# Performance work log

Hardware: AMD Instinct MI355X
Metric: run time of the kernel (lower is better)

## Reference

```python
import jax, jax.numpy as jnp
import numpy as np

N_NODES = 100000
N_EDGES = 3200000
IN_DIM, HID, OUT = 5, 64, 2


def _gcn_conv(x, W, b, src, dst):
    """PyG GCNConv: out = D^-1/2 (A + I) D^-1/2 (x W) + b.
    src/dst are edge_index[0]/edge_index[1] (source_to_target flow)."""
    n = x.shape[0]
    h = x @ W  # [N, out]
    # degree including self loop: deg[i] = 1 + #edges with dst == i
    deg = jnp.ones((n,), h.dtype).at[dst].add(1.0)
    inv_sqrt = jax.lax.rsqrt(deg)
    coef = inv_sqrt[src] * inv_sqrt[dst]  # [E]
    msgs = h[src] * coef[:, None]  # [E, out] gather
    agg = jax.ops.segment_sum(msgs, dst, num_segments=n)  # scatter-add
    # self-loop contribution: norm = inv_sqrt[i]^2 = 1/deg[i]
    agg = agg + h * (1.0 / deg)[:, None]
    return agg + b


def setup_inputs() -> dict:
    key = jax.random.key(0)
    ks = jax.random.split(key, 8)
    x = jax.random.normal(ks[0], (N_NODES, IN_DIM), dtype=jnp.float32)
    edge_index = jax.random.randint(ks[1], (2, N_EDGES), 0, N_NODES, dtype=jnp.int32)
    def glorot(k, fan_in, fan_out):
        lim = np.sqrt(6.0 / (fan_in + fan_out)).astype(np.float32)
        return jax.random.uniform(k, (fan_in, fan_out), jnp.float32, -lim, lim)
    return {
        "x": x,
        "edge_index": edge_index,
        "W1": glorot(ks[2], IN_DIM, HID), "b1": jnp.zeros((HID,), jnp.float32),
        "W2": glorot(ks[3], HID, HID),    "b2": jnp.zeros((HID,), jnp.float32),
        "W3": glorot(ks[4], HID, OUT),    "b3": jnp.zeros((OUT,), jnp.float32),
    }


def reference(x, edge_index, W1, b1, W2, b2, W3, b3):
    src, dst = edge_index[0], edge_index[1]
    # eval mode: dropout is identity
    h = jax.nn.relu(_gcn_conv(x, W1, b1, src, dst))
    h = jax.nn.relu(_gcn_conv(h, W2, b2, src, dst))
    return _gcn_conv(h, W3, b3, src, dst)
```

## Files before the change

### kernel.cpp

```cpp
#include <hip/hip_runtime.h>

#define CB 256
#define MAXNB 1024


__global__ void k_hist(const int* __restrict__ dst, int* __restrict__ histG,
                       int E, int NB, int chunk) {
  __shared__ int hist[MAXNB];
  int b = blockIdx.x, tid = threadIdx.x;
  for (int k = tid; k < NB; k += 256) hist[k] = 0;
  __syncthreads();
  int beg = b * chunk, end = min(E, beg + chunk);
  for (int i = beg + tid; i < end; i += 256) atomicAdd(&hist[dst[i] >> 8], 1);
  __syncthreads();
  for (int k = tid; k < NB; k += 256) histG[(size_t)k * CB + b] = hist[k];
}

__global__ void k_scan_local(const int* __restrict__ in, int* __restrict__ out,
                             int* __restrict__ blockSums, int n) {
  __shared__ int wsum[16];
  __shared__ int wpre[16];
  int tid = threadIdx.x;
  int gid = blockIdx.x * 1024 + tid;
  int v = (gid < n) ? in[gid] : 0;
  int lane = tid & 63, wv = tid >> 6;
  int x = v;
#pragma unroll
  for (int d = 1; d < 64; d <<= 1) {
    int t = __shfl_up(x, d);
    if (lane >= d) x += t;
  }
  if (lane == 63) wsum[wv] = x;
  __syncthreads();
  if (tid == 0) {
    int run = 0;
#pragma unroll
    for (int i = 0; i < 16; ++i) { wpre[i] = run; run += wsum[i]; }
    blockSums[blockIdx.x] = run;
  }
  __syncthreads();
  if (gid < n) out[gid] = x - v + wpre[wv];
}

__global__ void k_scan_blocks(const int* __restrict__ blockSums, int* __restrict__ blockOffs, int nb) {
  __shared__ int wtot[4];
  int tid = threadIdx.x;
  int lane = tid & 63, w = tid >> 6;
  int v = (tid < nb) ? blockSums[tid] : 0;
  int x = v;
#pragma unroll
  for (int d = 1; d < 64; d <<= 1) {
    int t = __shfl_up(x, d);
    if (lane >= d) x += t;
  }
  if (lane == 63) wtot[w] = x;
  __syncthreads();
  int pre = 0;
  for (int i = 0; i < w; ++i) pre += wtot[i];
  int ex = x - v + pre;
  if (tid < nb) blockOffs[tid] = ex;
  if (tid == nb - 1) blockOffs[nb] = ex + v;
}

__global__ void k_scatter(const int* __restrict__ src, const int* __restrict__ dst,
                          const int* __restrict__ histS, const int* __restrict__ blockOffs,
                          unsigned* __restrict__ recs, int E, int NB, int chunk) {
  __shared__ int cur[MAXNB];
  int b = blockIdx.x, tid = threadIdx.x;
  for (int k = tid; k < NB; k += 256) {
    int gid = k * CB + b;
    cur[k] = histS[gid] + blockOffs[gid >> 10];
  }
  __syncthreads();
  int beg = b * chunk, end = min(E, beg + chunk);
  for (int i = beg + tid; i < end; i += 256) {
    int s = src[i], d = dst[i];
    int pos = atomicAdd(&cur[d >> 8], 1);
    recs[pos] = ((unsigned)s << 8) | (unsigned)(d & 255);
  }
}

__global__ void k_build(const unsigned* __restrict__ recs, const int* __restrict__ histS,
                        const int* __restrict__ blockOffs,
                        int* __restrict__ offs, float* __restrict__ inv_sqrt,
                        int* __restrict__ srcs, int N, int NB, int E) {
  __shared__ int cnt[256];
  __shared__ int cur[256];
  __shared__ int wtot[4];
  int k = blockIdx.x, tid = threadIdx.x;
  int g0 = k * CB;
  int ebeg = histS[g0] + blockOffs[g0 >> 10];
  int eend = E;
  if (k + 1 < NB) {
    int g1 = (k + 1) * CB;
    eend = histS[g1] + blockOffs[g1 >> 10];
  }
  cnt[tid] = 0;
  __syncthreads();
  for (int i = ebeg + tid; i < eend; i += 256) atomicAdd(&cnt[recs[i] & 255u], 1);
  __syncthreads();
  int v = cnt[tid];
  int lane = tid & 63, w = tid >> 6;
  int x = v;
#pragma unroll
  for (int d = 1; d < 64; d <<= 1) {
    int t = __shfl_up(x, d);
    if (lane >= d) x += t;
  }
  if (lane == 63) wtot[w] = x;
  __syncthreads();
  int pre = 0;
  for (int i = 0; i < w; ++i) pre += wtot[i];
  int gpos = ebeg + (x - v) + pre;
  int node = k * 256 + tid;
  if (node < N) {
    offs[node] = gpos;
    inv_sqrt[node] = rsqrtf(1.0f + (float)v);
  }
  cur[tid] = gpos;
  if (k == NB - 1 && tid == 0) offs[N] = E;
  __syncthreads();
  for (int i = ebeg + tid; i < eend; i += 256) {
    unsigned r = recs[i];
    int pos = atomicAdd(&cur[r & 255u], 1);
    srcs[pos] = (int)(r >> 8);
  }
}


__global__ void k_l12(const float* __restrict__ x, const int* __restrict__ offs,
                      const int* __restrict__ srcs, const float* __restrict__ inv_sqrt,
                      const float* __restrict__ W1, const float* __restrict__ b1,
                      const float* __restrict__ W2, float* __restrict__ h2raw, int n) {
  __shared__ float hrow[4][2][64];
  int tid = threadIdx.x;
  int lane = tid & 63, w = tid >> 6;
  int hl = lane & 31, half = lane >> 5;
  float w1r[5];
#pragma unroll
  for (int k = 0; k < 5; ++k) w1r[k] = W1[k * 64 + lane];
  float bias = b1[lane];
  float wreg[64];
#pragma unroll
  for (int k = 0; k < 64; ++k) wreg[k] = W2[k * 64 + lane];
  float* slotA = &hrow[w][0][0];
  float* slotB = &hrow[w][1][0];
  int wid0 = (blockIdx.x * blockDim.x + tid) >> 6;
  int nw = (gridDim.x * blockDim.x) >> 6;
  for (int i2 = wid0 * 2; i2 < n; i2 += nw * 2) {
    int iA = i2, iB = i2 + 1;
    int node = (half == 0) ? iA : iB;
    bool valid = node < n;
    float a0 = 0.f, a1 = 0.f, a2 = 0.f, a3 = 0.f, a4 = 0.f;
    float isd = 0.f;
    if (valid) {
      isd = inv_sqrt[node];
      int beg = offs[node], end = offs[node + 1];
      for (int j = beg + hl; j < end; j += 32) {
        int s = srcs[j];
        float c = inv_sqrt[s] * isd;
        const float* xs = x + (size_t)s * 5;
        float4 xv = *(const float4*)xs;
        float x4 = xs[4];
        a0 = fmaf(xv.x, c, a0); a1 = fmaf(xv.y, c, a1); a2 = fmaf(xv.z, c, a2);
        a3 = fmaf(xv.w, c, a3); a4 = fmaf(x4, c, a4);
      }
    }
#pragma unroll
    for (int d = 16; d; d >>= 1) {
      a0 += __shfl_xor(a0, d); a1 += __shfl_xor(a1, d); a2 += __shfl_xor(a2, d);
      a3 += __shfl_xor(a3, d); a4 += __shfl_xor(a4, d);
    }
    if (valid) {
      float sc = isd * isd;
      const float* xi = x + (size_t)node * 5;
      a0 = fmaf(xi[0], sc, a0); a1 = fmaf(xi[1], sc, a1); a2 = fmaf(xi[2], sc, a2);
      a3 = fmaf(xi[3], sc, a3); a4 = fmaf(xi[4], sc, a4);
    }
    float aA0 = __shfl(a0, hl),      aA1 = __shfl(a1, hl),      aA2 = __shfl(a2, hl);
    float aA3 = __shfl(a3, hl),      aA4 = __shfl(a4, hl);
    float aB0 = __shfl(a0, hl | 32), aB1 = __shfl(a1, hl | 32), aB2 = __shfl(a2, hl | 32);
    float aB3 = __shfl(a3, hl | 32), aB4 = __shfl(a4, hl | 32);
    float hA = bias;
    hA = fmaf(aA0, w1r[0], hA); hA = fmaf(aA1, w1r[1], hA); hA = fmaf(aA2, w1r[2], hA);
    hA = fmaf(aA3, w1r[3], hA); hA = fmaf(aA4, w1r[4], hA);
    hA = fmaxf(hA, 0.f);
    float hB = bias;
    hB = fmaf(aB0, w1r[0], hB); hB = fmaf(aB1, w1r[1], hB); hB = fmaf(aB2, w1r[2], hB);
    hB = fmaf(aB3, w1r[3], hB); hB = fmaf(aB4, w1r[4], hB);
    hB = fmaxf(hB, 0.f);
    slotA[lane] = hA;
    slotB[lane] = hB;
    float ac0 = 0.f, ac1 = 0.f, ac2 = 0.f, ac3 = 0.f;
#pragma unroll
    for (int k4 = 0; k4 < 16; ++k4) {
      float4 hq = *(const float4*)&slotA[k4 * 4];
      ac0 = fmaf(hq.x, wreg[k4 * 4],     ac0);
      ac1 = fmaf(hq.y, wreg[k4 * 4 + 1], ac1);
      ac2 = fmaf(hq.z, wreg[k4 * 4 + 2], ac2);
      ac3 = fmaf(hq.w, wreg[k4 * 4 + 3], ac3);
    }
    h2raw[(size_t)iA * 64 + lane] = (ac0 + ac1) + (ac2 + ac3);
    if (iB < n) {
      float bc0 = 0.f, bc1 = 0.f, bc2 = 0.f, bc3 = 0.f;
#pragma unroll
      for (int k4 = 0; k4 < 16; ++k4) {
        float4 hq = *(const float4*)&slotB[k4 * 4];
        bc0 = fmaf(hq.x, wreg[k4 * 4],     bc0);
        bc1 = fmaf(hq.y, wreg[k4 * 4 + 1], bc1);
        bc2 = fmaf(hq.z, wreg[k4 * 4 + 2], bc2);
        bc3 = fmaf(hq.w, wreg[k4 * 4 + 3], bc3);
      }
      h2raw[(size_t)iB * 64 + lane] = (bc0 + bc1) + (bc2 + bc3);
    }
  }
}

__global__ void k_agg64w3(const float* __restrict__ hraw, const int* __restrict__ offs,
                          const int* __restrict__ srcs, const float* __restrict__ inv_sqrt,
                          const float* __restrict__ b2, const float* __restrict__ W3,
                          float* __restrict__ h3, int n) {
  int wid = (blockIdx.x * blockDim.x + threadIdx.x) >> 6;
  int lane = threadIdx.x & 63;
  if (wid >= n) return;
  int sub = lane >> 4;
  int fl  = lane & 15;
  float w30[4], w31[4];
#pragma unroll
  for (int q = 0; q < 4; ++q) {
    w30[q] = W3[(fl * 4 + q) * 2];
    w31[q] = W3[(fl * 4 + q) * 2 + 1];
  }
  int beg = offs[wid], end = offs[wid + 1];
  float isd = inv_sqrt[wid];
  float ax0 = 0.f, ay0 = 0.f, az0 = 0.f, aw0 = 0.f;
  float ax1 = 0.f, ay1 = 0.f, az1 = 0.f, aw1 = 0.f;
  int j = beg + sub;
  for (; j + 12 < end; j += 16) {
    int s0 = srcs[j], s1 = srcs[j + 4], s2 = srcs[j + 8], s3 = srcs[j + 12];
    float c0 = inv_sqrt[s0] * isd, c1 = inv_sqrt[s1] * isd;
    float c2 = inv_sqrt[s2] * isd, c3 = inv_sqrt[s3] * isd;
    float4 r0 = *(const float4*)(hraw + (size_t)s0 * 64 + fl * 4);
    float4 r1 = *(const float4*)(hraw + (size_t)s1 * 64 + fl * 4);
    float4 r2 = *(const float4*)(hraw + (size_t)s2 * 64 + fl * 4);
    float4 r3 = *(const float4*)(hraw + (size_t)s3 * 64 + fl * 4);
    ax0 = fmaf(r0.x, c0, ax0); ay0 = fmaf(r0.y, c0, ay0);
    az0 = fmaf(r0.z, c0, az0); aw0 = fmaf(r0.w, c0, aw0);
    ax1 = fmaf(r1.x, c1, ax1); ay1 = fmaf(r1.y, c1, ay1);
    az1 = fmaf(r1.z, c1, az1); aw1 = fmaf(r1.w, c1, aw1);
    ax0 = fmaf(r2.x, c2, ax0); ay0 = fmaf(r2.y, c2, ay0);
    az0 = fmaf(r2.z, c2, az0); aw0 = fmaf(r2.w, c2, aw0);
    ax1 = fmaf(r3.x, c3, ax1); ay1 = fmaf(r3.y, c3, ay1);
    az1 = fmaf(r3.z, c3, az1); aw1 = fmaf(r3.w, c3, aw1);
  }
  for (; j < end; j += 4) {
    int s0 = srcs[j];
    float c0 = inv_sqrt[s0] * isd;
    float4 r0 = *(const float4*)(hraw + (size_t)s0 * 64 + fl * 4);
    ax0 = fmaf(r0.x, c0, ax0); ay0 = fmaf(r0.y, c0, ay0);
    az0 = fmaf(r0.z, c0, az0); aw0 = fmaf(r0.w, c0, aw0);
  }
  float ax = ax0 + ax1, ay = ay0 + ay1, az = az0 + az1, aw = aw0 + aw1;
  ax += __shfl_xor(ax, 16); ay += __shfl_xor(ay, 16);
  az += __shfl_xor(az, 16); aw += __shfl_xor(aw, 16);
  ax += __shfl_xor(ax, 32); ay += __shfl_xor(ay, 32);
  az += __shfl_xor(az, 32); aw += __shfl_xor(aw, 32);
  float sc = isd * isd;
  float4 self = *(const float4*)(hraw + (size_t)wid * 64 + fl * 4);
  float4 bb   = *(const float4*)(b2 + fl * 4);
  float hx = fmaxf(ax + self.x * sc + bb.x, 0.f);
  float hy = fmaxf(ay + self.y * sc + bb.y, 0.f);
  float hz = fmaxf(az + self.z * sc + bb.z, 0.f);
  float hw = fmaxf(aw + self.w * sc + bb.w, 0.f);
  float p0 = hx * w30[0] + hy * w30[1] + hz * w30[2] + hw * w30[3];
  float p1 = hx * w31[0] + hy * w31[1] + hz * w31[2] + hw * w31[3];
#pragma unroll
  for (int d = 8; d; d >>= 1) { p0 += __shfl_xor(p0, d); p1 += __shfl_xor(p1, d); }
  if (lane == 0) {
    h3[(size_t)wid * 2]     = p0;
    h3[(size_t)wid * 2 + 1] = p1;
  }
}

__global__ void k_agg2(const float* __restrict__ h3, const int* __restrict__ offs,
                       const int* __restrict__ srcs, const float* __restrict__ inv_sqrt,
                       const float* __restrict__ b3, float* __restrict__ out, int n) {
  int wid = (blockIdx.x * blockDim.x + threadIdx.x) >> 6;
  int lane = threadIdx.x & 63;
  if (wid >= n) return;
  int beg = offs[wid], end = offs[wid + 1];
  float isd = inv_sqrt[wid];
  float a0 = 0.f, a1 = 0.f;
  for (int j = beg + lane; j < end; j += 64) {
    int s = srcs[j];
    float c = inv_sqrt[s] * isd;
    a0 = fmaf(h3[(size_t)s * 2], c, a0);
    a1 = fmaf(h3[(size_t)s * 2 + 1], c, a1);
  }
#pragma unroll
  for (int d = 32; d; d >>= 1) { a0 += __shfl_xor(a0, d); a1 += __shfl_xor(a1, d); }
  if (lane == 0) {
    float sc = isd * isd;
    out[(size_t)wid * 2]     = a0 + h3[(size_t)wid * 2] * sc + b3[0];
    out[(size_t)wid * 2 + 1] = a1 + h3[(size_t)wid * 2 + 1] * sc + b3[1];
  }
}


extern "C" void kernel_launch(void* const* d_in, const int* in_sizes, int n_in,
                              void* d_out, int out_size, void* d_ws, size_t ws_size,
                              hipStream_t stream) {
  const float* x  = (const float*)d_in[0];
  const int*   ei = (const int*)d_in[1];
  const float* W1 = (const float*)d_in[2];
  const float* b1 = (const float*)d_in[3];
  const float* W2 = (const float*)d_in[4];
  const float* b2 = (const float*)d_in[5];
  const float* W3 = (const float*)d_in[6];
  const float* b3 = (const float*)d_in[7];
  float* out = (float*)d_out;

  const int N = in_sizes[0] / 5;
  const int E = in_sizes[1] / 2;
  const int* src = ei;
  const int* dst = ei + E;

  const int NB = (N + 255) >> 8;
  const int chunk = (E + CB - 1) / CB;
  const int n2 = NB * CB;
  const int nb2 = (n2 + 1023) / 1024;

  char* p = (char*)d_ws;
  auto alloc = [&](size_t bytes) {
    char* r = p;
    p += (bytes + 255) & ~(size_t)255;
    return r;
  };
  int*      histG     = (int*)alloc((size_t)n2 * 4);
  int*      histS     = (int*)alloc((size_t)n2 * 4);
  int*      blockSums = (int*)alloc((size_t)nb2 * 4);
  int*      blockOffs = (int*)alloc((size_t)(nb2 + 1) * 4);
  unsigned* recs      = (unsigned*)alloc((size_t)E * 4);
  int*      srcs      = (int*)alloc((size_t)E * 4);
  int*      offs      = (int*)alloc((size_t)(N + 1) * 4);
  float*    inv_sqrt  = (float*)alloc((size_t)N * 4);
  float*    hB        = (float*)alloc((size_t)N * 64 * 4);
  float*    h3        = (float*)alloc((size_t)N * 2 * 4);

  const int wavesBlocks = (N * 64 + 255) / 256;

  k_hist<<<CB, 256, 0, stream>>>(dst, histG, E, NB, chunk);
  k_scan_local<<<nb2, 1024, 0, stream>>>(histG, histS, blockSums, n2);
  k_scan_blocks<<<1, 256, 0, stream>>>(blockSums, blockOffs, nb2);
  k_scatter<<<CB, 256, 0, stream>>>(src, dst, histS, blockOffs, recs, E, NB, chunk);
  k_build<<<NB, 256, 0, stream>>>(recs, histS, blockOffs, offs, inv_sqrt, srcs, N, NB, E);

  k_l12<<<2048, 256, 0, stream>>>(x, offs, srcs, inv_sqrt, W1, b1, W2, hB, N);
  k_agg64w3<<<wavesBlocks, 256, 0, stream>>>(hB, offs, srcs, inv_sqrt, b2, W3, h3, N);
  k_agg2<<<wavesBlocks, 256, 0, stream>>>(h3, offs, srcs, inv_sqrt, b3, out, N);
}
```

Baseline: 263.7 us.

## Pre-scale features by inv_sqrt and slice 64-wide hidden layer for aggregation

Source features are pre-multiplied by inv_sqrt(deg) in the build and GEMM epilogues, which removes the per-edge gather of inv_sqrt[s] in every aggregation. The 64-wide hidden layer is stored as eight feature slices of 8 floats each, and each block aggregates one slice. This keeps the gathered working set per slice small enough to stay cache-resident. Partial W3 projections per slice are then summed in a new small kernel. This adds an extra launch and a partial buffer, and the slice kernel reads srcs eight times.

```diff
diff --git a/kernel.cpp b/kernel.cpp
--- a/kernel.cpp
+++ b/kernel.cpp
@@ -81,9 +81,10 @@
 }
 
 __global__ void k_build(const unsigned* __restrict__ recs, const int* __restrict__ histS,
-                        const int* __restrict__ blockOffs,
+                        const int* __restrict__ blockOffs, const float* __restrict__ x,
                         int* __restrict__ offs, float* __restrict__ inv_sqrt,
-                        int* __restrict__ srcs, int N, int NB, int E) {
+                        float* __restrict__ xp, int* __restrict__ srcs,
+                        int N, int NB, int E) {
   __shared__ int cnt[256];
   __shared__ int cur[256];
   __shared__ int wtot[4];
@@ -101,21 +102,26 @@
   __syncthreads();
   int v = cnt[tid];
   int lane = tid & 63, w = tid >> 6;
-  int x = v;
+  int x_ = v;
 #pragma unroll
   for (int d = 1; d < 64; d <<= 1) {
-    int t = __shfl_up(x, d);
-    if (lane >= d) x += t;
-  }
-  if (lane == 63) wtot[w] = x;
+    int t = __shfl_up(x_, d);
+    if (lane >= d) x_ += t;
+  }
+  if (lane == 63) wtot[w] = x_;
   __syncthreads();
   int pre = 0;
   for (int i = 0; i < w; ++i) pre += wtot[i];
-  int gpos = ebeg + (x - v) + pre;
+  int gpos = ebeg + (x_ - v) + pre;
   int node = k * 256 + tid;
   if (node < N) {
     offs[node] = gpos;
-    inv_sqrt[node] = rsqrtf(1.0f + (float)v);
+    float is = rsqrtf(1.0f + (float)v);
+    inv_sqrt[node] = is;
+    const float* xr = x + (size_t)node * 5;
+    float* xo = xp + (size_t)node * 5;
+    xo[0] = xr[0] * is; xo[1] = xr[1] * is; xo[2] = xr[2] * is;
+    xo[3] = xr[3] * is; xo[4] = xr[4] * is;
   }
   cur[tid] = gpos;
   if (k == NB - 1 && tid == 0) offs[N] = E;
@@ -128,14 +134,15 @@
 }
 
 
-__global__ void k_l12(const float* __restrict__ x, const int* __restrict__ offs,
+__global__ void k_l12(const float* __restrict__ xp, const int* __restrict__ offs,
                       const int* __restrict__ srcs, const float* __restrict__ inv_sqrt,
                       const float* __restrict__ W1, const float* __restrict__ b1,
-                      const float* __restrict__ W2, float* __restrict__ h2raw, int n) {
+                      const float* __restrict__ W2, float* __restrict__ hS, int n) {
   __shared__ float hrow[4][2][64];
   int tid = threadIdx.x;
   int lane = tid & 63, w = tid >> 6;
   int hl = lane & 31, half = lane >> 5;
+  int slice = lane >> 3, feat = lane & 7;
   float w1r[5];
 #pragma unroll
   for (int k = 0; k < 5; ++k) w1r[k] = W1[k * 64 + lane];
@@ -158,12 +165,10 @@
       int beg = offs[node], end = offs[node + 1];
       for (int j = beg + hl; j < end; j += 32) {
         int s = srcs[j];
-        float c = inv_sqrt[s] * isd;
-        const float* xs = x + (size_t)s * 5;
+        const float* xs = xp + (size_t)s * 5;
         float4 xv = *(const float4*)xs;
         float x4 = xs[4];
-        a0 = fmaf(xv.x, c, a0); a1 = fmaf(xv.y, c, a1); a2 = fmaf(xv.z, c, a2);
-        a3 = fmaf(xv.w, c, a3); a4 = fmaf(x4, c, a4);
+        a0 += xv.x; a1 += xv.y; a2 += xv.z; a3 += xv.w; a4 += x4;
       }
     }
 #pragma unroll
@@ -172,15 +177,15 @@
       a3 += __shfl_xor(a3, d); a4 += __shfl_xor(a4, d);
     }
     if (valid) {
-      float sc = isd * isd;
-      const float* xi = x + (size_t)node * 5;
-      a0 = fmaf(xi[0], sc, a0); a1 = fmaf(xi[1], sc, a1); a2 = fmaf(xi[2], sc, a2);
-      a3 = fmaf(xi[3], sc, a3); a4 = fmaf(xi[4], sc, a4);
+      const float* xi = xp + (size_t)node * 5;
+      a0 = (a0 + xi[0]) * isd; a1 = (a1 + xi[1]) * isd; a2 = (a2 + xi[2]) * isd;
+      a3 = (a3 + xi[3]) * isd; a4 = (a4 + xi[4]) * isd;
     }
     float aA0 = __shfl(a0, hl),      aA1 = __shfl(a1, hl),      aA2 = __shfl(a2, hl);
     float aA3 = __shfl(a3, hl),      aA4 = __shfl(a4, hl);
     float aB0 = __shfl(a0, hl | 32), aB1 = __shfl(a1, hl | 32), aB2 = __shfl(a2, hl | 32);
     float aB3 = __shfl(a3, hl | 32), aB4 = __shfl(a4, hl | 32);
+    float isdA = __shfl(isd, 0), isdB = __shfl(isd, 32);
     float hA = bias;
     hA = fmaf(aA0, w1r[0], hA); hA = fmaf(aA1, w1r[1], hA); hA = fmaf(aA2, w1r[2], hA);
     hA = fmaf(aA3, w1r[3], hA); hA = fmaf(aA4, w1r[4], hA);
@@ -200,7 +205,7 @@
       ac2 = fmaf(hq.z, wreg[k4 * 4 + 2], ac2);
       ac3 = fmaf(hq.w, wreg[k4 * 4 + 3], ac3);
     }
-    h2raw[(size_t)iA * 64 + lane] = (ac0 + ac1) + (ac2 + ac3);
+    hS[((size_t)slice * n + iA) * 8 + feat] = ((ac0 + ac1) + (ac2 + ac3)) * isdA;
     if (iB < n) {
       float bc0 = 0.f, bc1 = 0.f, bc2 = 0.f, bc3 = 0.f;
 #pragma unroll
@@ -211,98 +216,86 @@
         bc2 = fmaf(hq.z, wreg[k4 * 4 + 2], bc2);
         bc3 = fmaf(hq.w, wreg[k4 * 4 + 3], bc3);
       }
-      h2raw[(size_t)iB * 64 + lane] = (bc0 + bc1) + (bc2 + bc3);
-    }
-  }
-}
-
-__global__ void k_agg64w3(const float* __restrict__ hraw, const int* __restrict__ offs,
-                          const int* __restrict__ srcs, const float* __restrict__ inv_sqrt,
-                          const float* __restrict__ b2, const float* __restrict__ W3,
-                          float* __restrict__ h3, int n) {
-  int wid = (blockIdx.x * blockDim.x + threadIdx.x) >> 6;
-  int lane = threadIdx.x & 63;
-  if (wid >= n) return;
-  int sub = lane >> 4;
-  int fl  = lane & 15;
-  float w30[4], w31[4];
-#pragma unroll
-  for (int q = 0; q < 4; ++q) {
-    w30[q] = W3[(fl * 4 + q) * 2];
-    w31[q] = W3[(fl * 4 + q) * 2 + 1];
-  }
-  int beg = offs[wid], end = offs[wid + 1];
-  float isd = inv_sqrt[wid];
-  float ax0 = 0.f, ay0 = 0.f, az0 = 0.f, aw0 = 0.f;
-  float ax1 = 0.f, ay1 = 0.f, az1 = 0.f, aw1 = 0.f;
-  int j = beg + sub;
-  for (; j + 12 < end; j += 16) {
-    int s0 = srcs[j], s1 = srcs[j + 4], s2 = srcs[j + 8], s3 = srcs[j + 12];
-    float c0 = inv_sqrt[s0] * isd, c1 = inv_sqrt[s1] * isd;
-    float c2 = inv_sqrt[s2] * isd, c3 = inv_sqrt[s3] * isd;
-    float4 r0 = *(const float4*)(hraw + (size_t)s0 * 64 + fl * 4);
-    float4 r1 = *(const float4*)(hraw + (size_t)s1 * 64 + fl * 4);
-    float4 r2 = *(const float4*)(hraw + (size_t)s2 * 64 + fl * 4);
-    float4 r3 = *(const float4*)(hraw + (size_t)s3 * 64 + fl * 4);
-    ax0 = fmaf(r0.x, c0, ax0); ay0 = fmaf(r0.y, c0, ay0);
-    az0 = fmaf(r0.z, c0, az0); aw0 = fmaf(r0.w, c0, aw0);
-    ax1 = fmaf(r1.x, c1, ax1); ay1 = fmaf(r1.y, c1, ay1);
-    az1 = fmaf(r1.z, c1, az1); aw1 = fmaf(r1.w, c1, aw1);
-    ax0 = fmaf(r2.x, c2, ax0); ay0 = fmaf(r2.y, c2, ay0);
-    az0 = fmaf(r2.z, c2, az0); aw0 = fmaf(r2.w, c2, aw0);
-    ax1 = fmaf(r3.x, c3, ax1); ay1 = fmaf(r3.y, c3, ay1);
-    az1 = fmaf(r3.z, c3, az1); aw1 = fmaf(r3.w, c3, aw1);
-  }
-  for (; j < end; j += 4) {
-    int s0 = srcs[j];
-    float c0 = inv_sqrt[s0] * isd;
-    float4 r0 = *(const float4*)(hraw + (size_t)s0 * 64 + fl * 4);
-    ax0 = fmaf(r0.x, c0, ax0); ay0 = fmaf(r0.y, c0, ay0);
-    az0 = fmaf(r0.z, c0, az0); aw0 = fmaf(r0.w, c0, aw0);
-  }
-  float ax = ax0 + ax1, ay = ay0 + ay1, az = az0 + az1, aw = aw0 + aw1;
-  ax += __shfl_xor(ax, 16); ay += __shfl_xor(ay, 16);
-  az += __shfl_xor(az, 16); aw += __shfl_xor(aw, 16);
-  ax += __shfl_xor(ax, 32); ay += __shfl_xor(ay, 32);
-  az += __shfl_xor(az, 32); aw += __shfl_xor(aw, 32);
-  float sc = isd * isd;
-  float4 self = *(const float4*)(hraw + (size_t)wid * 64 + fl * 4);
-  float4 bb   = *(const float4*)(b2 + fl * 4);
-  float hx = fmaxf(ax + self.x * sc + bb.x, 0.f);
-  float hy = fmaxf(ay + self.y * sc + bb.y, 0.f);
-  float hz = fmaxf(az + self.z * sc + bb.z, 0.f);
-  float hw = fmaxf(aw + self.w * sc + bb.w, 0.f);
-  float p0 = hx * w30[0] + hy * w30[1] + hz * w30[2] + hw * w30[3];
-  float p1 = hx * w31[0] + hy * w31[1] + hz * w31[2] + hw * w31[3];
-#pragma unroll
-  for (int d = 8; d; d >>= 1) { p0 += __shfl_xor(p0, d); p1 += __shfl_xor(p1, d); }
-  if (lane == 0) {
-    h3[(size_t)wid * 2]     = p0;
-    h3[(size_t)wid * 2 + 1] = p1;
-  }
-}
-
-__global__ void k_agg2(const float* __restrict__ h3, const int* __restrict__ offs,
+      hS[((size_t)slice * n + iB) * 8 + feat] = ((bc0 + bc1) + (bc2 + bc3)) * isdB;
+    }
+  }
+}
+
+__global__ void k_aggS(const float* __restrict__ hS, const int* __restrict__ offs,
+                       const int* __restrict__ srcs, const float* __restrict__ inv_sqrt,
+                       const float* __restrict__ b2, const float* __restrict__ W3,
+                       float* __restrict__ part, int n) {
+  int slice = blockIdx.x & 7;
+  int tid = threadIdx.x;
+  int lane = tid & 63;
+  int slot = lane >> 3, feat = lane & 7;
+  int f = slice * 8 + feat;
+  float b2v = b2[f];
+  float w30 = W3[f * 2], w31 = W3[f * 2 + 1];
+  const float* hbase = hS + (size_t)slice * n * 8;
+  int wid0 = ((blockIdx.x >> 3) << 2) + (tid >> 6);
+  int nw = (gridDim.x >> 3) << 2;
+  for (int i = wid0; i < n; i += nw) {
+    int beg = offs[i], end = offs[i + 1];
+    float acc0 = 0.f, acc1 = 0.f;
+    int j = beg + slot;
+    for (; j + 8 < end; j += 16) {
+      int s0 = srcs[j], s1 = srcs[j + 8];
+      acc0 += hbase[(size_t)s0 * 8 + feat];
+      acc1 += hbase[(size_t)s1 * 8 + feat];
+    }
+    if (j < end) acc0 += hbase[(size_t)srcs[j] * 8 + feat];
+    float selfv = hbase[(size_t)i * 8 + feat];
+    float acc = acc0 + acc1;
+    acc += __shfl_xor(acc, 8);
+    acc += __shfl_xor(acc, 16);
+    acc += __shfl_xor(acc, 32);
+    float isd = inv_sqrt[i];
+    float h2 = fmaxf(fmaf(isd, acc + selfv, b2v), 0.f);
+    float p0 = h2 * w30, p1 = h2 * w31;
+    p0 += __shfl_xor(p0, 1); p1 += __shfl_xor(p1, 1);
+    p0 += __shfl_xor(p0, 2); p1 += __shfl_xor(p1, 2);
+    p0 += __shfl_xor(p0, 4); p1 += __shfl_xor(p1, 4);
+    if (lane == 0) {
+      float2 pr; pr.x = p0; pr.y = p1;
+      *(float2*)(part + ((size_t)i * 8 + slice) * 2) = pr;
+    }
+  }
+}
+
+__global__ void k_sumpart(const float* __restrict__ part, const float* __restrict__ inv_sqrt,
+                          float* __restrict__ h3p, int n) {
+  int i = blockIdx.x * blockDim.x + threadIdx.x;
+  if (i >= n) return;
+  const float4* p = (const float4*)(part + (size_t)i * 16);
+  float4 q0 = p[0], q1 = p[1], q2 = p[2], q3 = p[3];
+  float is = inv_sqrt[i];
+  float s0 = ((q0.x + q0.z) + (q1.x + q1.z)) + ((q2.x + q2.z) + (q3.x + q3.z));
+  float s1 = ((q0.y + q0.w) + (q1.y + q1.w)) + ((q2.y + q2.w) + (q3.y + q3.w));
+  float2 r; r.x = s0 * is; r.y = s1 * is;
+  *(float2*)(h3p + (size_t)i * 2) = r;
+}
+
+__global__ void k_agg2(const float* __restrict__ h3p, const int* __restrict__ offs,
                        const int* __restrict__ srcs, const float* __restrict__ inv_sqrt,
                        const float* __restrict__ b3, float* __restrict__ out, int n) {
   int wid = (blockIdx.x * blockDim.x + threadIdx.x) >> 6;
   int lane = threadIdx.x & 63;
   if (wid >= n) return;
   int beg = offs[wid], end = offs[wid + 1];
-  float isd = inv_sqrt[wid];
   float a0 = 0.f, a1 = 0.f;
   for (int j = beg + lane; j < end; j += 64) {
     int s = srcs[j];
-    float c = inv_sqrt[s] * isd;
-    a0 = fmaf(h3[(size_t)s * 2], c, a0);
-    a1 = fmaf(h3[(size_t)s * 2 + 1], c, a1);
+    float2 hv = *(const float2*)(h3p + (size_t)s * 2);
+    a0 += hv.x; a1 += hv.y;
   }
 #pragma unroll
   for (int d = 32; d; d >>= 1) { a0 += __shfl_xor(a0, d); a1 += __shfl_xor(a1, d); }
   if (lane == 0) {
-    float sc = isd * isd;
-    out[(size_t)wid * 2]     = a0 + h3[(size_t)wid * 2] * sc + b3[0];
-    out[(size_t)wid * 2 + 1] = a1 + h3[(size_t)wid * 2 + 1] * sc + b3[1];
+    float isd = inv_sqrt[wid];
+    float2 self = *(const float2*)(h3p + (size_t)wid * 2);
+    out[(size_t)wid * 2]     = fmaf(isd, a0 + self.x, b3[0]);
+    out[(size_t)wid * 2 + 1] = fmaf(isd, a1 + self.y, b3[1]);
   }
 }
 
@@ -344,8 +337,10 @@
   int*      srcs      = (int*)alloc((size_t)E * 4);
   int*      offs      = (int*)alloc((size_t)(N + 1) * 4);
   float*    inv_sqrt  = (float*)alloc((size_t)N * 4);
-  float*    hB        = (float*)alloc((size_t)N * 64 * 4);
-  float*    h3        = (float*)alloc((size_t)N * 2 * 4);
+  float*    xp        = (float*)alloc((size_t)N * 5 * 4);
+  float*    hS        = (float*)alloc((size_t)N * 64 * 4);
+  float*    part      = (float*)alloc((size_t)N * 16 * 4);
+  float*    h3p       = (float*)alloc((size_t)N * 2 * 4);
 
   const int wavesBlocks = (N * 64 + 255) / 256;
 
@@ -353,9 +348,10 @@
   k_scan_local<<<nb2, 1024, 0, stream>>>(histG, histS, blockSums, n2);
   k_scan_blocks<<<1, 256, 0, stream>>>(blockSums, blockOffs, nb2);
   k_scatter<<<CB, 256, 0, stream>>>(src, dst, histS, blockOffs, recs, E, NB, chunk);
-  k_build<<<NB, 256, 0, stream>>>(recs, histS, blockOffs, offs, inv_sqrt, srcs, N, NB, E);
-
-  k_l12<<<2048, 256, 0, stream>>>(x, offs, srcs, inv_sqrt, W1, b1, W2, hB, N);
-  k_agg64w3<<<wavesBlocks, 256, 0, stream>>>(hB, offs, srcs, inv_sqrt, b2, W3, h3, N);
-  k_agg2<<<wavesBlocks, 256, 0, stream>>>(h3, offs, srcs, inv_sqrt, b3, out, N);
-}
+  k_build<<<NB, 256, 0, stream>>>(recs, histS, blockOffs, x, offs, inv_sqrt, xp, srcs, N, NB, E);
+
+  k_l12<<<2048, 256, 0, stream>>>(xp, offs, srcs, inv_sqrt, W1, b1, W2, hS, N);
+  k_aggS<<<2048, 256, 0, stream>>>(hS, offs, srcs, inv_sqrt, b2, W3, part, N);
+  k_sumpart<<<(N + 255) / 256, 256, 0, stream>>>(part, inv_sqrt, h3p, N);
+  k_agg2<<<wavesBlocks, 256, 0, stream>>>(h3p, offs, srcs, inv_sqrt, b3, out, N);
+}
```

Result: slower. 382.3 us (+45.0%).
